# Performance work log

Measured on AMD Instinct MI355X. Metric: run time of the kernel, lower is better.

## Reference

```python
import jax, jax.numpy as jnp
import numpy as np

MAX_RAY_LENGTH = 200.0


def setup_inputs() -> dict:
    key = jax.random.key(0)
    ks = jax.random.split(key, 6)
    D, K, R = 1296, 64, 16          # num_directions, num_points, rank
    F = 408                          # num_subcarriers
    return {
        "attenuation_real": jax.random.normal(ks[0], (D, K, R), dtype=jnp.float32),
        "attenuation_imag": jax.random.normal(ks[1], (D, K, R), dtype=jnp.float32),
        "radiation_real": jax.random.normal(ks[2], (D, K, R), dtype=jnp.float32),
        "radiation_imag": jax.random.normal(ks[3], (D, K, R), dtype=jnp.float32),
        "freq_real": jax.random.normal(ks[4], (F, R), dtype=jnp.float32),
        "freq_imag": jax.random.normal(ks[5], (F, R), dtype=jnp.float32),
    }


def reference(attenuation_real, attenuation_imag, radiation_real, radiation_imag,
              freq_real, freq_imag):
    # Complexify (complex64)
    att = jax.lax.complex(attenuation_real, attenuation_imag)   # (D, K, R)
    rad = jax.lax.complex(radiation_real, radiation_imag)       # (D, K, R)
    fbv = jax.lax.complex(freq_real, freq_imag)                 # (F, R)

    num_directions, num_points, _ = att.shape
    delta_t = MAX_RAY_LENGTH / num_points

    # u_hat_rho = cumsum over points of conj(att) * delta_t  (D, K, R)
    u_hat_rho = jnp.cumsum(jnp.conj(att) * delta_t, axis=1)

    # Factorized equivalent of the original rank^2 / rank^3 outer-product einsums:
    # einsum('rki,rkj->rkij', rad*, att*) contracted with einsum('fi,fj->fij', f, f)
    # == (rad* @ f^T) * (att* @ f^T) summed over i,j separately.
    p = jnp.einsum('rki,fi->rkf', jnp.conj(rad), fbv)           # (D, K, F)
    q = jnp.einsum('rki,fi->rkf', jnp.conj(att), fbv)           # (D, K, F)

    first_order = (p * q).sum(axis=1) * delta_t                  # (D, F)

    # Second order uses points [1:] and conj(u_hat_rho)
    h = jnp.einsum('rkl,fl->rkf', jnp.conj(u_hat_rho), fbv)     # (D, K, F)
    second_order = (p[:, 1:] * q[:, 1:] * h[:, 1:]).sum(axis=1) * delta_t  # (D, F)

    csi = (first_order + second_order).sum(axis=0) / num_directions  # (F,)
    return csi
```

## Files before the change

### kernel.cpp

```cpp
#include <hip/hip_runtime.h>

#define D_DIRS 1296
#define K_PTS  64
#define R_RANK 16
#define F_SUB  408
#define DT_VAL (200.0f / 64.0f)

#define NBLOCKS (D_DIRS / 2)
#define PARTIAL_FLOATS 8704
#define RED_CHUNKS 12
#define SLABS_PER_CHUNK (NBLOCKS / RED_CHUNKS)
#define NEED_BYTES ((size_t)(RED_CHUNKS + NBLOCKS) * PARTIAL_FLOATS * 4)
#define SKEW(e) ((e) + ((e) >> 5))

template <bool USE_PARTIALS>
__global__ __launch_bounds__(256, 4) void accum_kernel_t(
    const float* __restrict__ att_r, const float* __restrict__ att_i,
    const float* __restrict__ rad_r, const float* __restrict__ rad_i,
    float* __restrict__ pbuf, float* __restrict__ atomic_dst)
{
    __shared__ float4 sAtt4[2][K_PTS * 8];
    __shared__ float2 sRad2[2][K_PTS * R_RANK];

    const int t  = threadIdx.x;
    const int ri = t >> 4;
    const int rj = t & 15;

    for (int h = 0; h < 2; ++h) {
        const int base = (blockIdx.x * 2 + h) * K_PTS * R_RANK;
#pragma unroll
        for (int s = t; s < 512; s += 256) {
            float2 ar = *(const float2*)(att_r + base + 2 * s);
            float2 ai = *(const float2*)(att_i + base + 2 * s);
            sAtt4[h][s] = make_float4(ar.x, ai.x, ar.y, ai.y);
            float2 rr = *(const float2*)(rad_r + base + 2 * s);
            float2 rim = *(const float2*)(rad_i + base + 2 * s);
            sRad2[h][2 * s]     = make_float2(rr.x, rim.x);
            sRad2[h][2 * s + 1] = make_float2(rr.y, rim.y);
        }
    }
    __syncthreads();

    float accR[16], accI[16];
#pragma unroll
    for (int l = 0; l < 16; ++l) { accR[l] = 0.f; accI[l] = 0.f; }
    float gR = 0.f, gI = 0.f;

    for (int h = 0; h < 2; ++h) {
        const float2* rad2 = sRad2[h];
        const float2* att2 = (const float2*)sAtt4[h];
        const float4* att4 = sAtt4[h];

        float Sr = 0.f, Si = 0.f;
        for (int k = K_PTS - 1; k >= 1; --k) {
            float2 a = rad2[k * 16 + ri];
            float2 b = att2[k * 16 + rj];
            Sr += a.x * b.x - a.y * b.y;
            Si -= a.x * b.y + a.y * b.x;
#pragma unroll
            for (int q = 0; q < 8; ++q) {
                float4 c = att4[k * 8 + q];
                accR[2 * q]     += Sr * c.x - Si * c.y;
                accI[2 * q]     += Sr * c.y + Si * c.x;
                accR[2 * q + 1] += Sr * c.z - Si * c.w;
                accI[2 * q + 1] += Sr * c.w + Si * c.z;
            }
        }
#pragma unroll
        for (int q = 0; q < 8; ++q) {
            float4 c = att4[q];
            accR[2 * q]     += Sr * c.x - Si * c.y;
            accI[2 * q]     += Sr * c.y + Si * c.x;
            accR[2 * q + 1] += Sr * c.z - Si * c.w;
            accI[2 * q + 1] += Sr * c.w + Si * c.z;
        }
        float2 a0 = rad2[ri], b0 = att2[rj];
        gR += Sr + (a0.x * b0.x - a0.y * b0.y);
        gI += Si - (a0.x * b0.y + a0.y * b0.x);
    }

    if (USE_PARTIALS) {
        float4* slabT = (float4*)(pbuf + (size_t)blockIdx.x * PARTIAL_FLOATS);
#pragma unroll
        for (int v = 0; v < 8; ++v) {
            slabT[t * 8 + v] = make_float4(
                accR[2 * v] * DT_VAL,     accI[2 * v] * DT_VAL,
                accR[2 * v + 1] * DT_VAL, accI[2 * v + 1] * DT_VAL);
        }
        float2* slabG = (float2*)(pbuf + (size_t)blockIdx.x * PARTIAL_FLOATS + 8192);
        slabG[t] = make_float2(gR, gI);
    } else {
#pragma unroll
        for (int l = 0; l < 16; ++l) {
            atomicAdd(&atomic_dst[(t * 16 + l) * 2 + 0], accR[l] * DT_VAL);
            atomicAdd(&atomic_dst[(t * 16 + l) * 2 + 1], accI[l] * DT_VAL);
        }
        atomicAdd(&atomic_dst[8192 + t * 2 + 0], gR);
        atomicAdd(&atomic_dst[8192 + t * 2 + 1], gI);
    }
}

__global__ __launch_bounds__(256) void reduce1_kernel(
    const float* __restrict__ pbuf, float* __restrict__ red1)
{
    int e = blockIdx.x * 256 + threadIdx.x;
    const float* p = pbuf + (size_t)blockIdx.y * SLABS_PER_CHUNK * PARTIAL_FLOATS + e;
    float s = 0.f;
#pragma unroll 6
    for (int b = 0; b < SLABS_PER_CHUNK; ++b)
        s += p[(size_t)b * PARTIAL_FLOATS];
    red1[blockIdx.y * PARTIAL_FLOATS + e] = s;
}

__global__ __launch_bounds__(256) void contract_kernel(
    const float* __restrict__ fr, const float* __restrict__ fi,
    const float* __restrict__ red1, float* __restrict__ out)
{
    __shared__ float sTG[PARTIAL_FLOATS + PARTIAL_FLOATS / 32];
    __shared__ float sfr[16], sfi[16];

    const int f = blockIdx.x;
    const int t = threadIdx.x;

    for (int e = t; e < PARTIAL_FLOATS; e += 256) {
        float s = 0.f;
#pragma unroll
        for (int c = 0; c < RED_CHUNKS; ++c)
            s += red1[c * PARTIAL_FLOATS + e];
        sTG[SKEW(e)] = s;
    }
    if (t < 16) {
        sfr[t] = fr[f * R_RANK + t];
        sfi[t] = fi[f * R_RANK + t];
    }
    __syncthreads();

    const int i = t >> 4, j = t & 15;
    float fir = sfr[i], fii = sfi[i];
    float fjr = sfr[j], fji = sfi[j];
    float mr = fir * fjr - fii * fji;
    float mi = fir * fji + fii * fjr;

    int gbase = 8192 + t * 2;
    float Sr = sTG[SKEW(gbase)];
    float Si = sTG[SKEW(gbase + 1)];
#pragma unroll
    for (int l = 0; l < 16; ++l) {
        int e0 = (t * 16 + l) * 2;
        float Tr = sTG[SKEW(e0)];
        float Ti = sTG[SKEW(e0 + 1)];
        float flr = sfr[l], fli = sfi[l];
        Sr += Tr * flr - Ti * fli;
        Si += Tr * fli + Ti * flr;
    }

    float vr = Sr * mr - Si * mi;
    float vi = Sr * mi + Si * mr;

#pragma unroll
    for (int off = 32; off >= 1; off >>= 1) {
        vr += __shfl_down(vr, off, 64);
        vi += __shfl_down(vi, off, 64);
    }
    __shared__ float red[8];
    const int lane = t & 63, w = t >> 6;
    if (lane == 0) { red[w * 2] = vr; red[w * 2 + 1] = vi; }
    __syncthreads();
    if (t == 0) {
        float rr = red[0] + red[2] + red[4] + red[6];
        float ii = red[1] + red[3] + red[5] + red[7];
        const float scale = DT_VAL / (float)D_DIRS;
        out[f]         = rr * scale;
        out[F_SUB + f] = ii * scale;
    }
}

extern "C" void kernel_launch(void* const* d_in, const int* in_sizes, int n_in,
                              void* d_out, int out_size, void* d_ws, size_t ws_size,
                              hipStream_t stream)
{
    const float* att_r = (const float*)d_in[0];
    const float* att_i = (const float*)d_in[1];
    const float* rad_r = (const float*)d_in[2];
    const float* rad_i = (const float*)d_in[3];
    const float* fr    = (const float*)d_in[4];
    const float* fi    = (const float*)d_in[5];

    float* ws   = (float*)d_ws;
    float* red1 = ws;
    float* pbuf = ws + RED_CHUNKS * PARTIAL_FLOATS;

    const bool use_partials = ws_size >= NEED_BYTES;

    if (use_partials) {
        accum_kernel_t<true><<<NBLOCKS, 256, 0, stream>>>(
            att_r, att_i, rad_r, rad_i, pbuf, red1);
        reduce1_kernel<<<dim3(PARTIAL_FLOATS / 256, RED_CHUNKS), 256, 0, stream>>>(
            pbuf, red1);
    } else {
        hipMemsetAsync(red1, 0, RED_CHUNKS * PARTIAL_FLOATS * sizeof(float), stream);
        accum_kernel_t<false><<<NBLOCKS, 256, 0, stream>>>(
            att_r, att_i, rad_r, rad_i, pbuf, red1);
    }

    contract_kernel<<<F_SUB, 256, 0, stream>>>(
        fr, fi, red1, (float*)d_out);
}
```

Before: 168.7 us.

## Split directions across half-blocks with 2-row register tiles and LDS merge

Each thread now handles two (i,j) rows for a single direction instead of one row across both directions. The two 128-thread halves process the two directions in parallel, and their partial sums are merged through LDS reused via a union. This reuses each att4 LDS load for two rows and halves the sequential k-loop length per thread. In exchange it doubles accumulator registers, lowers the occupancy hint from 4 to 2, and adds extra barriers for the merge.

```diff
diff --git a/kernel.cpp b/kernel.cpp
--- a/kernel.cpp
+++ b/kernel.cpp
@@ -13,90 +13,145 @@
 #define NEED_BYTES ((size_t)(RED_CHUNKS + NBLOCKS) * PARTIAL_FLOATS * 4)
 #define SKEW(e) ((e) + ((e) >> 5))
 
+union SMem {
+    struct {
+        float4 att4[2][K_PTS * 8];
+        float2 rad2[2][K_PTS * R_RANK];
+    } tiles;
+    float4 mrgT[2048];
+};
+
 template <bool USE_PARTIALS>
-__global__ __launch_bounds__(256, 4) void accum_kernel_t(
+__global__ __launch_bounds__(256, 2) void accum_kernel_t(
     const float* __restrict__ att_r, const float* __restrict__ att_i,
     const float* __restrict__ rad_r, const float* __restrict__ rad_i,
     float* __restrict__ pbuf, float* __restrict__ atomic_dst)
 {
-    __shared__ float4 sAtt4[2][K_PTS * 8];
-    __shared__ float2 sRad2[2][K_PTS * R_RANK];
+    __shared__ SMem sm;
 
     const int t  = threadIdx.x;
-    const int ri = t >> 4;
-    const int rj = t & 15;
-
-    for (int h = 0; h < 2; ++h) {
-        const int base = (blockIdx.x * 2 + h) * K_PTS * R_RANK;
+    const int h  = t >> 7;
+    const int t2 = t & 127;
+    const int i0 = t2 >> 4;
+    const int i1 = i0 + 8;
+    const int j  = t2 & 15;
+
+    for (int hh = 0; hh < 2; ++hh) {
+        const int base = (blockIdx.x * 2 + hh) * (K_PTS * R_RANK);
 #pragma unroll
         for (int s = t; s < 512; s += 256) {
             float2 ar = *(const float2*)(att_r + base + 2 * s);
             float2 ai = *(const float2*)(att_i + base + 2 * s);
-            sAtt4[h][s] = make_float4(ar.x, ai.x, ar.y, ai.y);
+            sm.tiles.att4[hh][s] = make_float4(ar.x, ai.x, ar.y, ai.y);
             float2 rr = *(const float2*)(rad_r + base + 2 * s);
-            float2 rim = *(const float2*)(rad_i + base + 2 * s);
-            sRad2[h][2 * s]     = make_float2(rr.x, rim.x);
-            sRad2[h][2 * s + 1] = make_float2(rr.y, rim.y);
-        }
-    }
-    __syncthreads();
-
-    float accR[16], accI[16];
-#pragma unroll
-    for (int l = 0; l < 16; ++l) { accR[l] = 0.f; accI[l] = 0.f; }
-    float gR = 0.f, gI = 0.f;
-
-    for (int h = 0; h < 2; ++h) {
-        const float2* rad2 = sRad2[h];
-        const float2* att2 = (const float2*)sAtt4[h];
-        const float4* att4 = sAtt4[h];
-
-        float Sr = 0.f, Si = 0.f;
-        for (int k = K_PTS - 1; k >= 1; --k) {
-            float2 a = rad2[k * 16 + ri];
-            float2 b = att2[k * 16 + rj];
-            Sr += a.x * b.x - a.y * b.y;
-            Si -= a.x * b.y + a.y * b.x;
+            float2 rm = *(const float2*)(rad_i + base + 2 * s);
+            sm.tiles.rad2[hh][2 * s]     = make_float2(rr.x, rm.x);
+            sm.tiles.rad2[hh][2 * s + 1] = make_float2(rr.y, rm.y);
+        }
+    }
+    __syncthreads();
+
+    const float4* att4 = sm.tiles.att4[h];
+    const float2* att2 = (const float2*)att4;
+    const float2* rad2 = sm.tiles.rad2[h];
+
+    float aR0[16], aI0[16], aR1[16], aI1[16];
+#pragma unroll
+    for (int l = 0; l < 16; ++l) { aR0[l] = aI0[l] = aR1[l] = aI1[l] = 0.f; }
+    float S0r = 0.f, S0i = 0.f, S1r = 0.f, S1i = 0.f;
+
+    for (int k = K_PTS - 1; k >= 1; --k) {
+        float2 a0 = rad2[k * 16 + i0];
+        float2 a1 = rad2[k * 16 + i1];
+        float2 b  = att2[k * 16 + j];
+        S0r += a0.x * b.x - a0.y * b.y;   S0i -= a0.x * b.y + a0.y * b.x;
+        S1r += a1.x * b.x - a1.y * b.y;   S1i -= a1.x * b.y + a1.y * b.x;
+#pragma unroll
+        for (int q = 0; q < 8; ++q) {
+            float4 c = att4[k * 8 + q];
+            aR0[2*q]   += S0r * c.x - S0i * c.y;
+            aI0[2*q]   += S0r * c.y + S0i * c.x;
+            aR0[2*q+1] += S0r * c.z - S0i * c.w;
+            aI0[2*q+1] += S0r * c.w + S0i * c.z;
+            aR1[2*q]   += S1r * c.x - S1i * c.y;
+            aI1[2*q]   += S1r * c.y + S1i * c.x;
+            aR1[2*q+1] += S1r * c.z - S1i * c.w;
+            aI1[2*q+1] += S1r * c.w + S1i * c.z;
+        }
+    }
+#pragma unroll
+    for (int q = 0; q < 8; ++q) {
+        float4 c = att4[q];
+        aR0[2*q]   += S0r * c.x - S0i * c.y;
+        aI0[2*q]   += S0r * c.y + S0i * c.x;
+        aR0[2*q+1] += S0r * c.z - S0i * c.w;
+        aI0[2*q+1] += S0r * c.w + S0i * c.z;
+        aR1[2*q]   += S1r * c.x - S1i * c.y;
+        aI1[2*q]   += S1r * c.y + S1i * c.x;
+        aR1[2*q+1] += S1r * c.z - S1i * c.w;
+        aI1[2*q+1] += S1r * c.w + S1i * c.z;
+    }
+    {
+        float2 a0 = rad2[i0], a1 = rad2[i1], b0 = att2[j];
+        S0r += a0.x * b0.x - a0.y * b0.y;   S0i -= a0.x * b0.y + a0.y * b0.x;
+        S1r += a1.x * b0.x - a1.y * b0.y;   S1i -= a1.x * b0.y + a1.y * b0.x;
+    }
+
+    const int r0 = t2;
+    const int r1 = t2 + 128;
+
+    __syncthreads();
+
+    if (USE_PARTIALS) {
+        if (h == 1) {
 #pragma unroll
             for (int q = 0; q < 8; ++q) {
-                float4 c = att4[k * 8 + q];
-                accR[2 * q]     += Sr * c.x - Si * c.y;
-                accI[2 * q]     += Sr * c.y + Si * c.x;
-                accR[2 * q + 1] += Sr * c.z - Si * c.w;
-                accI[2 * q + 1] += Sr * c.w + Si * c.z;
+                sm.mrgT[r0 * 8 + ((q + r0) & 7)] =
+                    make_float4(aR0[2*q], aI0[2*q], aR0[2*q+1], aI0[2*q+1]);
+                sm.mrgT[r1 * 8 + ((q + r1) & 7)] =
+                    make_float4(aR1[2*q], aI1[2*q], aR1[2*q+1], aI1[2*q+1]);
             }
         }
-#pragma unroll
-        for (int q = 0; q < 8; ++q) {
-            float4 c = att4[q];
-            accR[2 * q]     += Sr * c.x - Si * c.y;
-            accI[2 * q]     += Sr * c.y + Si * c.x;
-            accR[2 * q + 1] += Sr * c.z - Si * c.w;
-            accI[2 * q + 1] += Sr * c.w + Si * c.z;
-        }
-        float2 a0 = rad2[ri], b0 = att2[rj];
-        gR += Sr + (a0.x * b0.x - a0.y * b0.y);
-        gI += Si - (a0.x * b0.y + a0.y * b0.x);
-    }
-
-    if (USE_PARTIALS) {
-        float4* slabT = (float4*)(pbuf + (size_t)blockIdx.x * PARTIAL_FLOATS);
-#pragma unroll
-        for (int v = 0; v < 8; ++v) {
-            slabT[t * 8 + v] = make_float4(
-                accR[2 * v] * DT_VAL,     accI[2 * v] * DT_VAL,
-                accR[2 * v + 1] * DT_VAL, accI[2 * v + 1] * DT_VAL);
-        }
-        float2* slabG = (float2*)(pbuf + (size_t)blockIdx.x * PARTIAL_FLOATS + 8192);
-        slabG[t] = make_float2(gR, gI);
+        __syncthreads();
+        if (h == 0) {
+            float4* slabT = (float4*)(pbuf + (size_t)blockIdx.x * PARTIAL_FLOATS);
+#pragma unroll
+            for (int q = 0; q < 8; ++q) {
+                float4 o0 = sm.mrgT[r0 * 8 + ((q + r0) & 7)];
+                slabT[r0 * 8 + q] = make_float4(
+                    (aR0[2*q]   + o0.x) * DT_VAL, (aI0[2*q]   + o0.y) * DT_VAL,
+                    (aR0[2*q+1] + o0.z) * DT_VAL, (aI0[2*q+1] + o0.w) * DT_VAL);
+                float4 o1 = sm.mrgT[r1 * 8 + ((q + r1) & 7)];
+                slabT[r1 * 8 + q] = make_float4(
+                    (aR1[2*q]   + o1.x) * DT_VAL, (aI1[2*q]   + o1.y) * DT_VAL,
+                    (aR1[2*q+1] + o1.z) * DT_VAL, (aI1[2*q+1] + o1.w) * DT_VAL);
+            }
+        }
+        __syncthreads();
+        float2* mrgG = (float2*)sm.mrgT;
+        if (h == 1) {
+            mrgG[r0] = make_float2(S0r, S0i);
+            mrgG[r1] = make_float2(S1r, S1i);
+        }
+        __syncthreads();
+        if (h == 0) {
+            float2* slabG = (float2*)(pbuf + (size_t)blockIdx.x * PARTIAL_FLOATS + 8192);
+            float2 o0 = mrgG[r0], o1 = mrgG[r1];
+            slabG[r0] = make_float2(S0r + o0.x, S0i + o0.y);
+            slabG[r1] = make_float2(S1r + o1.x, S1i + o1.y);
+        }
     } else {
 #pragma unroll
         for (int l = 0; l < 16; ++l) {
-            atomicAdd(&atomic_dst[(t * 16 + l) * 2 + 0], accR[l] * DT_VAL);
-            atomicAdd(&atomic_dst[(t * 16 + l) * 2 + 1], accI[l] * DT_VAL);
-        }
-        atomicAdd(&atomic_dst[8192 + t * 2 + 0], gR);
-        atomicAdd(&atomic_dst[8192 + t * 2 + 1], gI);
+            atomicAdd(&atomic_dst[(r0 * 16 + l) * 2 + 0], aR0[l] * DT_VAL);
+            atomicAdd(&atomic_dst[(r0 * 16 + l) * 2 + 1], aI0[l] * DT_VAL);
+            atomicAdd(&atomic_dst[(r1 * 16 + l) * 2 + 0], aR1[l] * DT_VAL);
+            atomicAdd(&atomic_dst[(r1 * 16 + l) * 2 + 1], aI1[l] * DT_VAL);
+        }
+        atomicAdd(&atomic_dst[8192 + r0 * 2 + 0], S0r);
+        atomicAdd(&atomic_dst[8192 + r0 * 2 + 1], S0i);
+        atomicAdd(&atomic_dst[8192 + r1 * 2 + 0], S1r);
+        atomicAdd(&atomic_dst[8192 + r1 * 2 + 1], S1i);
     }
 }
 
```

Result: no change. 168.4 us (-0.1%).

## Use packed FMA inner loop and split final reduction into separate kernel

Applied to the files above, without the earlier changes.

The accumulation inner loop now uses v_pk_fma_f32 inline assembly on float2 accumulators, with the attenuation values read as wave-uniform scalar operands straight from global memory instead of from shared memory. The 12-chunk reduction moves out of the contract kernel into a new reduce2 kernel, so each of the 408 contract blocks no longer re-reduces all chunks into shared memory. The intent is to halve VALU instruction count in the hot loop and remove redundant per-block reduction work. In exchange it adds a kernel launch, relies on the compiler placing the uniform loads in SGPRs for the "s" constraint, and drops the occupancy hint from launch_bounds.

```diff
diff --git a/kernel.cpp b/kernel.cpp
--- a/kernel.cpp
+++ b/kernel.cpp
@@ -10,90 +10,115 @@
 #define PARTIAL_FLOATS 8704
 #define RED_CHUNKS 12
 #define SLABS_PER_CHUNK (NBLOCKS / RED_CHUNKS)
-#define NEED_BYTES ((size_t)(RED_CHUNKS + NBLOCKS) * PARTIAL_FLOATS * 4)
-#define SKEW(e) ((e) + ((e) >> 5))
+#define NEED_BYTES ((size_t)(1 + RED_CHUNKS + NBLOCKS) * PARTIAL_FLOATS * 4)
+
+#define PK(acc, m, s) \
+    asm("v_pk_fma_f32 %0, %1, %2, %0" : "+v"(acc) : "v"(m), "s"(s))
 
 template <bool USE_PARTIALS>
-__global__ __launch_bounds__(256, 4) void accum_kernel_t(
+__global__ __launch_bounds__(256) void accum_kernel_t(
     const float* __restrict__ att_r, const float* __restrict__ att_i,
     const float* __restrict__ rad_r, const float* __restrict__ rad_i,
     float* __restrict__ pbuf, float* __restrict__ atomic_dst)
 {
-    __shared__ float4 sAtt4[2][K_PTS * 8];
-    __shared__ float2 sRad2[2][K_PTS * R_RANK];
-
-    const int t  = threadIdx.x;
-    const int ri = t >> 4;
-    const int rj = t & 15;
+    __shared__ float2 sAtt[2][K_PTS * R_RANK];
+    __shared__ float2 sRad[2][K_PTS * R_RANK];
+
+    const int t = threadIdx.x;
+    const int i = t >> 4;
+    const int j = t & 15;
 
     for (int h = 0; h < 2; ++h) {
-        const int base = (blockIdx.x * 2 + h) * K_PTS * R_RANK;
+        const int base = (blockIdx.x * 2 + h) * (K_PTS * R_RANK);
 #pragma unroll
         for (int s = t; s < 512; s += 256) {
             float2 ar = *(const float2*)(att_r + base + 2 * s);
             float2 ai = *(const float2*)(att_i + base + 2 * s);
-            sAtt4[h][s] = make_float4(ar.x, ai.x, ar.y, ai.y);
+            sAtt[h][2 * s]     = make_float2(ar.x, ai.x);
+            sAtt[h][2 * s + 1] = make_float2(ar.y, ai.y);
             float2 rr = *(const float2*)(rad_r + base + 2 * s);
-            float2 rim = *(const float2*)(rad_i + base + 2 * s);
-            sRad2[h][2 * s]     = make_float2(rr.x, rim.x);
-            sRad2[h][2 * s + 1] = make_float2(rr.y, rim.y);
+            float2 rm = *(const float2*)(rad_i + base + 2 * s);
+            sRad[h][2 * s]     = make_float2(rr.x, rm.x);
+            sRad[h][2 * s + 1] = make_float2(rr.y, rm.y);
         }
     }
     __syncthreads();
 
-    float accR[16], accI[16];
-#pragma unroll
-    for (int l = 0; l < 16; ++l) { accR[l] = 0.f; accI[l] = 0.f; }
+    float2 accR[8], accI[8];
+#pragma unroll
+    for (int q = 0; q < 8; ++q) {
+        accR[q] = make_float2(0.f, 0.f);
+        accI[q] = make_float2(0.f, 0.f);
+    }
     float gR = 0.f, gI = 0.f;
 
     for (int h = 0; h < 2; ++h) {
-        const float2* rad2 = sRad2[h];
-        const float2* att2 = (const float2*)sAtt4[h];
-        const float4* att4 = sAtt4[h];
+        const float2* A2 = sAtt[h];
+        const float2* R2 = sRad[h];
+        const float*  gre = att_r + (blockIdx.x * 2 + h) * (K_PTS * R_RANK);
+        const float*  gim = att_i + (blockIdx.x * 2 + h) * (K_PTS * R_RANK);
 
         float Sr = 0.f, Si = 0.f;
         for (int k = K_PTS - 1; k >= 1; --k) {
-            float2 a = rad2[k * 16 + ri];
-            float2 b = att2[k * 16 + rj];
+            float2 a = R2[k * 16 + i];
+            float2 b = A2[k * 16 + j];
             Sr += a.x * b.x - a.y * b.y;
             Si -= a.x * b.y + a.y * b.x;
-#pragma unroll
-            for (int q = 0; q < 8; ++q) {
-                float4 c = att4[k * 8 + q];
-                accR[2 * q]     += Sr * c.x - Si * c.y;
-                accI[2 * q]     += Sr * c.y + Si * c.x;
-                accR[2 * q + 1] += Sr * c.z - Si * c.w;
-                accI[2 * q + 1] += Sr * c.w + Si * c.z;
+            float2 SrP = make_float2(Sr, Sr);
+            float2 SiP = make_float2(Si, Si);
+            float2 SiN = make_float2(-Si, -Si);
+            const float4* re4 = (const float4*)(gre + k * 16);
+            const float4* im4 = (const float4*)(gim + k * 16);
+#pragma unroll
+            for (int q = 0; q < 4; ++q) {
+                float4 re = re4[q], im = im4[q];
+                float2 reL = make_float2(re.x, re.y), reH = make_float2(re.z, re.w);
+                float2 imL = make_float2(im.x, im.y), imH = make_float2(im.z, im.w);
+                PK(accR[2 * q],     SrP, reL);  PK(accR[2 * q],     SiN, imL);
+                PK(accR[2 * q + 1], SrP, reH);  PK(accR[2 * q + 1], SiN, imH);
+                PK(accI[2 * q],     SrP, imL);  PK(accI[2 * q],     SiP, reL);
+                PK(accI[2 * q + 1], SrP, imH);  PK(accI[2 * q + 1], SiP, reH);
             }
         }
-#pragma unroll
-        for (int q = 0; q < 8; ++q) {
-            float4 c = att4[q];
-            accR[2 * q]     += Sr * c.x - Si * c.y;
-            accI[2 * q]     += Sr * c.y + Si * c.x;
-            accR[2 * q + 1] += Sr * c.z - Si * c.w;
-            accI[2 * q + 1] += Sr * c.w + Si * c.z;
-        }
-        float2 a0 = rad2[ri], b0 = att2[rj];
-        gR += Sr + (a0.x * b0.x - a0.y * b0.y);
-        gI += Si - (a0.x * b0.y + a0.y * b0.x);
+        {
+            float2 SrP = make_float2(Sr, Sr);
+            float2 SiP = make_float2(Si, Si);
+            float2 SiN = make_float2(-Si, -Si);
+            const float4* re4 = (const float4*)gre;
+            const float4* im4 = (const float4*)gim;
+#pragma unroll
+            for (int q = 0; q < 4; ++q) {
+                float4 re = re4[q], im = im4[q];
+                float2 reL = make_float2(re.x, re.y), reH = make_float2(re.z, re.w);
+                float2 imL = make_float2(im.x, im.y), imH = make_float2(im.z, im.w);
+                PK(accR[2 * q],     SrP, reL);  PK(accR[2 * q],     SiN, imL);
+                PK(accR[2 * q + 1], SrP, reH);  PK(accR[2 * q + 1], SiN, imH);
+                PK(accI[2 * q],     SrP, imL);  PK(accI[2 * q],     SiP, reL);
+                PK(accI[2 * q + 1], SrP, imH);  PK(accI[2 * q + 1], SiP, reH);
+            }
+            float2 a0 = R2[i], b0 = A2[j];
+            gR += Sr + (a0.x * b0.x - a0.y * b0.y);
+            gI += Si - (a0.x * b0.y + a0.y * b0.x);
+        }
     }
 
     if (USE_PARTIALS) {
         float4* slabT = (float4*)(pbuf + (size_t)blockIdx.x * PARTIAL_FLOATS);
 #pragma unroll
-        for (int v = 0; v < 8; ++v) {
-            slabT[t * 8 + v] = make_float4(
-                accR[2 * v] * DT_VAL,     accI[2 * v] * DT_VAL,
-                accR[2 * v + 1] * DT_VAL, accI[2 * v + 1] * DT_VAL);
+        for (int q = 0; q < 8; ++q) {
+            slabT[t * 8 + q] = make_float4(
+                accR[q].x * DT_VAL, accI[q].x * DT_VAL,
+                accR[q].y * DT_VAL, accI[q].y * DT_VAL);
         }
         float2* slabG = (float2*)(pbuf + (size_t)blockIdx.x * PARTIAL_FLOATS + 8192);
         slabG[t] = make_float2(gR, gI);
     } else {
 #pragma unroll
-        for (int l = 0; l < 16; ++l) {
-            atomicAdd(&atomic_dst[(t * 16 + l) * 2 + 0], accR[l] * DT_VAL);
-            atomicAdd(&atomic_dst[(t * 16 + l) * 2 + 1], accI[l] * DT_VAL);
+        for (int q = 0; q < 8; ++q) {
+            atomicAdd(&atomic_dst[(t * 16 + 2 * q) * 2 + 0], accR[q].x * DT_VAL);
+            atomicAdd(&atomic_dst[(t * 16 + 2 * q) * 2 + 1], accI[q].x * DT_VAL);
+            atomicAdd(&atomic_dst[(t * 16 + 2 * q + 1) * 2 + 0], accR[q].y * DT_VAL);
+            atomicAdd(&atomic_dst[(t * 16 + 2 * q + 1) * 2 + 1], accI[q].y * DT_VAL);
         }
         atomicAdd(&atomic_dst[8192 + t * 2 + 0], gR);
         atomicAdd(&atomic_dst[8192 + t * 2 + 1], gI);
@@ -112,43 +137,45 @@
     red1[blockIdx.y * PARTIAL_FLOATS + e] = s;
 }
 
+__global__ __launch_bounds__(256) void reduce2_kernel(
+    const float* __restrict__ red1, float* __restrict__ TG_out)
+{
+    int e = blockIdx.x * 256 + threadIdx.x;
+    float s = 0.f;
+#pragma unroll
+    for (int c = 0; c < RED_CHUNKS; ++c)
+        s += red1[c * PARTIAL_FLOATS + e];
+    TG_out[e] = s;
+}
+
 __global__ __launch_bounds__(256) void contract_kernel(
     const float* __restrict__ fr, const float* __restrict__ fi,
-    const float* __restrict__ red1, float* __restrict__ out)
-{
-    __shared__ float sTG[PARTIAL_FLOATS + PARTIAL_FLOATS / 32];
-    __shared__ float sfr[16], sfi[16];
-
+    const float* __restrict__ T_ws, const float* __restrict__ G_ws,
+    float* __restrict__ out)
+{
     const int f = blockIdx.x;
     const int t = threadIdx.x;
-
-    for (int e = t; e < PARTIAL_FLOATS; e += 256) {
-        float s = 0.f;
-#pragma unroll
-        for (int c = 0; c < RED_CHUNKS; ++c)
-            s += red1[c * PARTIAL_FLOATS + e];
-        sTG[SKEW(e)] = s;
-    }
+    const int i = t >> 4;
+    const int j = t & 15;
+
+    __shared__ float sfr[16], sfi[16];
     if (t < 16) {
         sfr[t] = fr[f * R_RANK + t];
         sfi[t] = fi[f * R_RANK + t];
     }
     __syncthreads();
 
-    const int i = t >> 4, j = t & 15;
     float fir = sfr[i], fii = sfi[i];
     float fjr = sfr[j], fji = sfi[j];
     float mr = fir * fjr - fii * fji;
     float mi = fir * fji + fii * fjr;
 
-    int gbase = 8192 + t * 2;
-    float Sr = sTG[SKEW(gbase)];
-    float Si = sTG[SKEW(gbase + 1)];
+    float Sr = G_ws[t * 2 + 0];
+    float Si = G_ws[t * 2 + 1];
 #pragma unroll
     for (int l = 0; l < 16; ++l) {
-        int e0 = (t * 16 + l) * 2;
-        float Tr = sTG[SKEW(e0)];
-        float Ti = sTG[SKEW(e0 + 1)];
+        float Tr = T_ws[(t * 16 + l) * 2 + 0];
+        float Ti = T_ws[(t * 16 + l) * 2 + 1];
         float flr = sfr[l], fli = sfi[l];
         Sr += Tr * flr - Ti * fli;
         Si += Tr * fli + Ti * flr;
@@ -187,22 +214,24 @@
     const float* fi    = (const float*)d_in[5];
 
     float* ws   = (float*)d_ws;
-    float* red1 = ws;
-    float* pbuf = ws + RED_CHUNKS * PARTIAL_FLOATS;
+    float* TG   = ws;
+    float* red1 = ws + PARTIAL_FLOATS;
+    float* pbuf = ws + (1 + RED_CHUNKS) * PARTIAL_FLOATS;
 
     const bool use_partials = ws_size >= NEED_BYTES;
 
     if (use_partials) {
         accum_kernel_t<true><<<NBLOCKS, 256, 0, stream>>>(
-            att_r, att_i, rad_r, rad_i, pbuf, red1);
+            att_r, att_i, rad_r, rad_i, pbuf, TG);
         reduce1_kernel<<<dim3(PARTIAL_FLOATS / 256, RED_CHUNKS), 256, 0, stream>>>(
             pbuf, red1);
+        reduce2_kernel<<<PARTIAL_FLOATS / 256, 256, 0, stream>>>(red1, TG);
     } else {
-        hipMemsetAsync(red1, 0, RED_CHUNKS * PARTIAL_FLOATS * sizeof(float), stream);
+        hipMemsetAsync(TG, 0, PARTIAL_FLOATS * sizeof(float), stream);
         accum_kernel_t<false><<<NBLOCKS, 256, 0, stream>>>(
-            att_r, att_i, rad_r, rad_i, pbuf, red1);
+            att_r, att_i, rad_r, rad_i, pbuf, TG);
     }
 
     contract_kernel<<<F_SUB, 256, 0, stream>>>(
-        fr, fi, red1, (float*)d_out);
-}
+        fr, fi, TG, TG + 8192, (float*)d_out);
+}
```

Measured after the change: 198.5 us. +17.7%, slower.
